# Performance work log

Measured on AMD Instinct MI355X. Metric: run time of the kernel, lower is better.

The kernel has to match this reference:

```python
import jax, jax.numpy as jnp
import numpy as np

WINDOW = (7, 7, 7)
DIM = 192
HEADS = 6
B_ = 256
NW = 32
N = int(np.prod(WINDOW))


def _relative_position_index(window_size):
    coords = np.stack(np.meshgrid(*[np.arange(w) for w in window_size], indexing='ij'))
    cf = coords.reshape(len(window_size), -1)  # (3, N)
    rel = cf[:, :, None] - cf[:, None, :]      # (3, N, N)
    rel = rel.transpose(1, 2, 0).copy()        # (N, N, 3)
    for i, w in enumerate(window_size):
        rel[:, :, i] += w - 1
    rel[:, :, 0] *= (2 * window_size[1] - 1) * (2 * window_size[2] - 1)
    rel[:, :, 1] *= 2 * window_size[2] - 1
    return rel.sum(-1).astype(np.int32)       # (N, N)


def setup_inputs() -> dict:
    key = jax.random.key(0)
    ks = jax.random.split(key, 8)
    table_rows = int(np.prod([2 * w - 1 for w in WINDOW]))  # 2197
    s = 0.02
    return {
        'skip': jax.random.normal(ks[0], (B_, N, DIM), jnp.float32),
        'x_up': jax.random.normal(ks[1], (B_, N, DIM), jnp.float32),
        'mask': jax.random.normal(ks[2], (NW, N, N), jnp.float32),
        'rel_index': jnp.asarray(_relative_position_index(WINDOW)),
        'table': s * jax.random.normal(ks[3], (table_rows, HEADS), jnp.float32),
        'kv_w': jax.random.normal(ks[4], (DIM, 2 * DIM), jnp.float32) / np.sqrt(DIM),
        'kv_b': jnp.zeros((2 * DIM,), jnp.float32),
        'proj_w': jax.random.normal(ks[5], (DIM, DIM), jnp.float32) / np.sqrt(DIM),
        'proj_b': jnp.zeros((DIM,), jnp.float32),
    }


def reference(skip, x_up, mask, rel_index, table, kv_w, kv_b, proj_w, proj_b):
    B, n, C = skip.shape
    H = HEADS
    D = C // H
    scale = D ** -0.5
    # kv projection: (B, N, 2C) -> k, v each (B, H, N, D)
    kv = skip @ kv_w + kv_b
    kv = kv.reshape(B, n, 2, H, D)
    k = kv[:, :, 0].transpose(0, 2, 1, 3)
    v = kv[:, :, 1].transpose(0, 2, 1, 3)
    q = (x_up.reshape(B, n, H, D).transpose(0, 2, 1, 3)) * scale
    attn = jnp.einsum('bhnd,bhmd->bhnm', q, k)  # (B, H, N, N)
    # gathered relative position bias: (N, N, H) -> (H, N, N)
    bias = table[rel_index].transpose(2, 0, 1)
    attn = attn + bias[None]
    nW = mask.shape[0]
    attn = attn.reshape(B // nW, nW, H, n, n) + mask[None, :, None]
    attn = jax.nn.softmax(attn.reshape(B, H, n, n), axis=-1)
    x = jnp.einsum('bhnm,bhmd->bhnd', attn, v)
    x = x.transpose(0, 2, 1, 3).reshape(B, n, C)
    return x @ proj_w + proj_b
```

## Files before the change

kernel.cpp:

```cpp
#include <hip/hip_runtime.h>
#include <hip/hip_bf16.h>

#define B_  256
#define N_  343
#define C_  192
#define H_  6
#define D_  32
#define NW_ 32
#define NN_ (N_*N_)
#define TROWS 2197
#define NP_ 352
#define PLANE (NP_*NP_)

typedef unsigned int  uint32;
typedef unsigned short u16;
typedef __attribute__((ext_vector_type(8))) short bf16x8;
typedef __attribute__((ext_vector_type(4))) float f32x4;

union frag8 { uint4 u4; bf16x8 h8; short s[8]; };

__device__ __forceinline__ float bf2f(u16 u){
  union { uint32 u; float f; } v; v.u = ((uint32)u) << 16; return v.f;
}
__device__ __forceinline__ u16 f2bf(float f){
  union { float f; uint32 u; } v; v.f = f;
  uint32 u = v.u;
  return (u16)((u + 0x7FFFu + ((u >> 16) & 1u)) >> 16);
}

__device__ __forceinline__ bool detect_f32(const uint32* w){
  int c = 0;
  #pragma unroll
  for (int u = 0; u < 32; u++){
    int e = (w[u*37] >> 7) & 0xFF;
    c += (e > 150);
  }
  return c >= 3;
}
__device__ __forceinline__ float ldf(const void* p, size_t i, bool f32){
  return f32 ? ((const float*)p)[i] : bf2f(((const u16*)p)[i]);
}
__device__ __forceinline__ void stf(void* p, size_t i, float v, bool f32){
  if (f32) ((float*)p)[i] = v;
  else     ((u16*)p)[i]   = f2bf(v);
}

__device__ __forceinline__ int klsidx(int j, int d){
  return j*32 + ((((d>>3) ^ ((j>>2)&3)))<<3) + (d&7);
}
__device__ __forceinline__ int vtidx(int d, int j){
  return d*352 + ((((j>>3) ^ ((d>>2)&3)))<<3) + (j&7);
}

__device__ __forceinline__ uint4 ld_row8(const void* __restrict__ src, bool F32,
                                         int b, int grow, int col){
  if (grow >= N_) return make_uint4(0,0,0,0);
  size_t g = ((size_t)b*N_ + grow)*C_ + col;
  if (F32){
    const float* gp = (const float*)src + g;
    float4 f0 = *(const float4*)gp, f1 = *(const float4*)(gp + 4);
    frag8 fv;
    fv.s[0]=(short)f2bf(f0.x); fv.s[1]=(short)f2bf(f0.y);
    fv.s[2]=(short)f2bf(f0.z); fv.s[3]=(short)f2bf(f0.w);
    fv.s[4]=(short)f2bf(f1.x); fv.s[5]=(short)f2bf(f1.y);
    fv.s[6]=(short)f2bf(f1.z); fv.s[7]=(short)f2bf(f1.w);
    return fv.u4;
  }
  return *(const uint4*)((const u16*)src + g);
}


__global__ void prep_bp(const void* __restrict__ skip, const int* __restrict__ rel,
                        const void* __restrict__ table, u16* __restrict__ bp){
  const bool F32 = detect_f32((const uint32*)skip);
  size_t gid = ((size_t)blockIdx.x*256 + threadIdx.x)*8;
  int p   = (int)(gid / PLANE);
  int rem = (int)(gid % PLANE);
  int i = rem / NP_, j0 = rem % NP_;
  frag8 o;
  #pragma unroll
  for (int m = 0; m < 8; m++){
    int j = j0 + m; float v = 0.f;
    if (i < N_ && j < N_){
      int r = rel[i*N_ + j];
      v = ldf(table, (size_t)r*H_ + p, F32);
    }
    o.s[m] = (short)f2bf(v);
  }
  *(uint4*)&bp[gid] = o.u4;
}

__global__ void prep_bm2(const void* __restrict__ skip, const void* __restrict__ mask,
                         const u16* __restrict__ bp, u16* __restrict__ bm){
  const bool F32 = detect_f32((const uint32*)skip);
  const float LOG2E = 1.4426950408889634f;
  size_t gid = ((size_t)blockIdx.x*256 + threadIdx.x)*8;
  int pl  = (int)(gid / PLANE);
  int rem = (int)(gid % PLANE);
  int i = rem / NP_, j0 = rem % NP_;
  int w = pl / H_, h = pl % H_;
  frag8 bg; bg.u4 = *(const uint4*)&bp[(size_t)h*PLANE + rem];
  frag8 o;
  #pragma unroll
  for (int m = 0; m < 8; m++){
    int j = j0 + m;
    float v = bf2f((u16)bg.s[m]);
    if (i < N_ && j < N_) v += ldf(mask, (size_t)w*NN_ + (size_t)i*N_ + j, F32);
    o.s[m] = (short)f2bf(v * LOG2E);
  }
  *(uint4*)&bm[gid] = o.u4;
}

__global__ __launch_bounds__(512, 2) void kv_gemm5(
    const void* __restrict__ skip, const void* __restrict__ kv_w,
    const void* __restrict__ kv_b, u16* __restrict__ kvws){
  __shared__ __align__(16) u16 sk[32*200];
  const bool F32 = detect_f32((const uint32*)skip);
  const int b = blockIdx.x;
  const int t = threadIdx.x, lane = t & 63, wave = t >> 6;
  const int n16 = lane & 15, q = lane >> 4;

  float kvb[3];
  u16*  p3[3];
  int   d3[3], isK[3];
  frag8 bw[3][6];
  #pragma unroll
  for (int c3 = 0; c3 < 3; c3++){
    int col = (wave*3 + c3)*16 + n16;
    kvb[c3] = ldf(kv_b, col, F32);
    #pragma unroll
    for (int ks = 0; ks < 6; ks++)
      #pragma unroll
      for (int j = 0; j < 8; j++)
        bw[c3][ks].s[j] = (short)f2bf(ldf(kv_w, (size_t)(ks*32 + q*8 + j)*384 + col, F32));
    if (col < 192){
      int h = col >> 5; d3[c3] = col & 31; isK[c3] = 1;
      p3[c3] = kvws + (size_t)(b*H_ + h)*22528;
    } else {
      int cv = col - 192; int h = cv >> 5; d3[c3] = cv & 31; isK[c3] = 0;
      p3[c3] = kvws + (size_t)(b*H_ + h)*22528 + 11264;
    }
  }

  const int r0 = t/24,        c0 = (t%24)*8;
  const int r1 = (t+512)/24,  c1 = ((t+512)%24)*8;
  const bool two = (t < 256);
  uint4 pre0 = ld_row8(skip, F32, b, r0, c0);
  uint4 pre1 = two ? ld_row8(skip, F32, b, r1, c1) : make_uint4(0,0,0,0);

  for (int rc = 0; rc < 11; rc++){
    __syncthreads();
    *(uint4*)&sk[r0*200 + c0] = pre0;
    if (two) *(uint4*)&sk[r1*200 + c1] = pre1;
    __syncthreads();
    if (rc < 10){
      int rb = (rc+1)*32;
      pre0 = ld_row8(skip, F32, b, rb + r0, c0);
      if (two) pre1 = ld_row8(skip, F32, b, rb + r1, c1);
    }
    frag8 af[2][6];
    #pragma unroll
    for (int half = 0; half < 2; half++)
      #pragma unroll
      for (int ks = 0; ks < 6; ks++)
        af[half][ks].u4 = *(const uint4*)&sk[(half*16 + n16)*200 + ks*32 + q*8];
    #pragma unroll
    for (int c3 = 0; c3 < 3; c3++){
      #pragma unroll
      for (int half = 0; half < 2; half++){
        f32x4 acc = {0.f,0.f,0.f,0.f};
        #pragma unroll
        for (int ks = 0; ks < 6; ks++)
          acc = __builtin_amdgcn_mfma_f32_16x16x32_bf16(af[half][ks].h8, bw[c3][ks].h8, acc, 0,0,0);
        #pragma unroll
        for (int r = 0; r < 4; r++){
          int grow = rc*32 + half*16 + q*4 + r;
          u16 val = f2bf(acc[r] + kvb[c3]);
          if (isK[c3]) p3[c3][klsidx(grow, d3[c3])] = val;
          else         p3[c3][vtidx(d3[c3], grow)] = val;
        }
      }
    }
  }
}

#define A2_VT  11264
#define A2_TOT 22528

__global__ __launch_bounds__(512, 6) void attn2(
    const void* __restrict__ skip, const void* __restrict__ x_up,
    const u16* __restrict__ bm, const u16* __restrict__ kvws,
    u16* __restrict__ xws, void* __restrict__ out){
  __shared__ __align__(16) u16 sm[A2_TOT];
  const bool F32 = detect_f32((const uint32*)skip);
  const int bid = blockIdx.x;
  const int b = bid / H_, h = bid % H_;
  const int w = b & (NW_-1);
  const int t = threadIdx.x, lane = t & 63, wave = t >> 6;
  const int n16 = lane & 15, q = lane >> 4;

  {
    const uint4* src = (const uint4*)(kvws + (size_t)bid*22528);
    uint4* dst = (uint4*)sm;
    for (int u = t; u < 2816; u += 512) dst[u] = src[u];
  }
  __syncthreads();

  const u16* bmp = bm + (size_t)(w*H_ + h)*PLANE;
  const float SC2 = 0.17677669529663687f * 1.4426950408889634f;
  const int src0 = ((q & 1) << 5) + n16;
  const int src1 = src0 + 16;
  const bool lo = (q < 2);

  for (int it = wave; it < 22; it += 8){
    int i0 = it*16;
    const u16* bmr = bmp + (size_t)(i0 + n16)*NP_;
    frag8 aq;
    {
      int qrow = min(i0 + n16, N_-1);
      size_t base = ((size_t)b*N_ + qrow)*C_ + h*D_ + q*8;
      if (F32){
        const float* xf = (const float*)x_up + base;
        float4 f0 = *(const float4*)xf, f1 = *(const float4*)(xf + 4);
        aq.s[0]=(short)f2bf(f0.x); aq.s[1]=(short)f2bf(f0.y);
        aq.s[2]=(short)f2bf(f0.z); aq.s[3]=(short)f2bf(f0.w);
        aq.s[4]=(short)f2bf(f1.x); aq.s[5]=(short)f2bf(f1.y);
        aq.s[6]=(short)f2bf(f1.z); aq.s[7]=(short)f2bf(f1.w);
      } else {
        aq.u4 = *(const uint4*)((const u16*)x_up + base);
      }
    }
    f32x4 O0 = {0.f,0.f,0.f,0.f}, O1 = {0.f,0.f,0.f,0.f};
    float lp = 0.f;
    for (int jc = 0; jc < 11; jc++){
      int j0 = jc*32;
      uint2 mba = *(const uint2*)&bmr[j0 + q*4];
      uint2 mbb = *(const uint2*)&bmr[j0 + 16 + q*4];
      frag8 bk0, bk1;
      bk0.u4 = *(const uint4*)&sm[klsidx(j0 + n16, q*8)];
      bk1.u4 = *(const uint4*)&sm[klsidx(j0 + 16 + n16, q*8)];
      f32x4 z = {0.f,0.f,0.f,0.f};
      f32x4 s0 = __builtin_amdgcn_mfma_f32_16x16x32_bf16(bk0.h8, aq.h8, z, 0,0,0);
      f32x4 s1 = __builtin_amdgcn_mfma_f32_16x16x32_bf16(bk1.h8, aq.h8, z, 0,0,0);
      union { uint2 v; u16 e[4]; } Ua, Ub;
      Ua.v = mba; Ub.v = mbb;
      float pa[4], pb[4];
      if (jc < 10){
        #pragma unroll
        for (int r = 0; r < 4; r++){
          pa[r] = exp2f(fmaf(s0[r], SC2, bf2f(Ua.e[r])));
          pb[r] = exp2f(fmaf(s1[r], SC2, bf2f(Ub.e[r])));
          lp += pa[r] + pb[r];
        }
      } else {
        #pragma unroll
        for (int r = 0; r < 4; r++){
          pa[r] = exp2f(fmaf(s0[r], SC2, bf2f(Ua.e[r])));
          float eb = exp2f(fmaf(s1[r], SC2, bf2f(Ub.e[r])));
          pb[r] = (336 + q*4 + r < N_) ? eb : 0.f;
          lp += pa[r] + pb[r];
        }
      }
      uint32 A0, A1, B0, B1;
      asm("v_cvt_pk_bf16_f32 %0, %1, %2" : "=v"(A0) : "v"(pa[0]), "v"(pa[1]));
      asm("v_cvt_pk_bf16_f32 %0, %1, %2" : "=v"(A1) : "v"(pa[2]), "v"(pa[3]));
      asm("v_cvt_pk_bf16_f32 %0, %1, %2" : "=v"(B0) : "v"(pb[0]), "v"(pb[1]));
      asm("v_cvt_pk_bf16_f32 %0, %1, %2" : "=v"(B1) : "v"(pb[2]), "v"(pb[3]));
      uint32 a0s = (uint32)__shfl((int)A0, src0), a1s = (uint32)__shfl((int)A1, src0);
      uint32 a2s = (uint32)__shfl((int)A0, src1), a3s = (uint32)__shfl((int)A1, src1);
      uint32 b0s = (uint32)__shfl((int)B0, src0), b1s = (uint32)__shfl((int)B1, src0);
      uint32 b2s = (uint32)__shfl((int)B0, src1), b3s = (uint32)__shfl((int)B1, src1);
      frag8 ap;
      ap.u4.x = lo ? a0s : b0s;
      ap.u4.y = lo ? a1s : b1s;
      ap.u4.z = lo ? a2s : b2s;
      ap.u4.w = lo ? a3s : b3s;
      frag8 bv0, bv1;
      bv0.u4 = *(const uint4*)&sm[A2_VT + vtidx(n16,      j0 + q*8)];
      bv1.u4 = *(const uint4*)&sm[A2_VT + vtidx(16 + n16, j0 + q*8)];
      O0 = __builtin_amdgcn_mfma_f32_16x16x32_bf16(ap.h8, bv0.h8, O0, 0,0,0);
      O1 = __builtin_amdgcn_mfma_f32_16x16x32_bf16(ap.h8, bv1.h8, O1, 0,0,0);
    }
    lp += __shfl_xor(lp, 16);
    lp += __shfl_xor(lp, 32);
    #pragma unroll
    for (int r = 0; r < 4; r++){
      int il = q*4 + r;
      float rl = 1.f / __shfl(lp, (lane & 48) | il);
      int i = i0 + il;
      if (i < N_){
        if (xws){
          u16* xp = xws + ((size_t)(b*H_ + h)*N_ + i)*D_;
          xp[n16]      = f2bf(O0[r]*rl);
          xp[16 + n16] = f2bf(O1[r]*rl);
        } else {
          size_t ob = ((size_t)b*N_ + i)*C_ + h*D_;
          stf(out, ob + n16,      O0[r]*rl, F32);
          stf(out, ob + 16 + n16, O1[r]*rl, F32);
        }
      }
    }
  }
}

__global__ __launch_bounds__(256, 4) void proj4(const u16* __restrict__ xws,
                                                void* __restrict__ outp,
                                                const void* __restrict__ pw,
                                                const void* __restrict__ pb,
                                                const void* __restrict__ skip){
  __shared__ __align__(16) u16 xs[64*200];
  __shared__ __align__(16) float os[16*196];
  const bool F32 = detect_f32((const uint32*)skip);
  const int t = threadIdx.x, lane = t & 63, wave = t >> 6;
  const int n16 = lane & 15, q = lane >> 4;
  const size_t row0 = (size_t)blockIdx.x * 64;

  for (int u = t; u < 1536; u += 256){
    int r = u / 24, c8 = u % 24;
    int g = (int)row0 + r;
    int b = g / N_, i = g - b*N_;
    int h = c8 >> 2, d0 = (c8 & 3)*8;
    uint4 vv = *(const uint4*)&xws[((size_t)(b*H_ + h)*N_ + i)*D_ + d0];
    *(uint4*)&xs[r*200 + h*32 + d0] = vv;
  }
  frag8 bwf[3][6];
  float pbv[3];
  #pragma unroll
  for (int c3 = 0; c3 < 3; c3++){
    int col = (wave*3 + c3)*16 + n16;
    pbv[c3] = ldf(pb, col, F32);
    #pragma unroll
    for (int ks = 0; ks < 6; ks++)
      #pragma unroll
      for (int j = 0; j < 8; j++)
        bwf[c3][ks].s[j] = (short)f2bf(ldf(pw, (size_t)(ks*32 + q*8 + j)*C_ + col, F32));
  }
  __syncthreads();
  for (int rt = 0; rt < 4; rt++){
    frag8 af[6];
    #pragma unroll
    for (int ks = 0; ks < 6; ks++)
      af[ks].u4 = *(const uint4*)&xs[(rt*16 + n16)*200 + ks*32 + q*8];
    #pragma unroll
    for (int c3 = 0; c3 < 3; c3++){
      f32x4 acc = {0.f,0.f,0.f,0.f};
      #pragma unroll
      for (int ks = 0; ks < 6; ks++)
        acc = __builtin_amdgcn_mfma_f32_16x16x32_bf16(af[ks].h8, bwf[c3][ks].h8, acc, 0,0,0);
      int col = (wave*3 + c3)*16 + n16;
      #pragma unroll
      for (int r = 0; r < 4; r++)
        os[(q*4 + r)*196 + col] = acc[r] + pbv[c3];
    }
    __syncthreads();
    size_t rb = row0 + rt*16;
    if (F32){
      for (int u = t; u < 768; u += 256){
        int r = u / 48, c4 = (u % 48)*4;
        *(float4*)((float*)outp + (rb + r)*C_ + c4) = *(const float4*)&os[r*196 + c4];
      }
    } else {
      for (int u = t; u < 384; u += 256){
        int r = u / 24, c8 = (u % 24)*8;
        frag8 o;
        #pragma unroll
        for (int m = 0; m < 8; m++) o.s[m] = (short)f2bf(os[r*196 + c8 + m]);
        *(uint4*)((u16*)outp + (rb + r)*C_ + c8) = o.u4;
      }
    }
    __syncthreads();
  }
}


__global__ void prep_biasg(const void* __restrict__ skip, const int* __restrict__ rel,
                           const void* __restrict__ table, u16* __restrict__ biasg){
  const bool F32 = detect_f32((const uint32*)skip);
  int idx = blockIdx.x*256 + threadIdx.x;
  if (idx >= NN_) return;
  int r = rel[idx];
  #pragma unroll
  for (int h = 0; h < H_; h++)
    biasg[(size_t)h*NN_ + idx] = f2bf(ldf(table, (size_t)r*H_ + h, F32));
}

#define KLS_OFF 6400
#define VT_OFF  (KLS_OFF + 352*40)
#define SMEM_U16 (VT_OFF + 32*360)

__global__ __launch_bounds__(512, 4) void attn_fused(
    const void* __restrict__ skip, const void* __restrict__ x_up,
    const void* __restrict__ mask, const u16* __restrict__ biasg,
    const void* __restrict__ kv_w, const void* __restrict__ kv_b,
    void* __restrict__ out){
  __shared__ __align__(16) u16 sm[SMEM_U16];
  const bool F32 = detect_f32((const uint32*)skip);
  const int bid = blockIdx.x;
  const int b = bid / H_, h = bid % H_;
  const int w = b & (NW_-1);
  const int t = threadIdx.x;
  const int lane = t & 63, wave = t >> 6;
  const int n16 = lane & 15, q = lane >> 4;
  const int colt = wave & 3;
  const int half = wave >> 2;
  const int gcol = (colt < 2) ? (h*D_ + colt*16 + n16)
                              : (C_ + h*D_ + (colt-2)*16 + n16);
  const float kvb = ldf(kv_b, gcol, F32);
  frag8 bw[6];
  #pragma unroll
  for (int ks = 0; ks < 6; ks++)
    #pragma unroll
    for (int j = 0; j < 8; j++)
      bw[ks].s[j] = (short)f2bf(ldf(kv_w, (size_t)(ks*32 + q*8 + j)*384 + gcol, F32));

  for (int rc = 0; rc < 11; rc++){
    __syncthreads();
    for (int u = t; u < 32*C_; u += 512){
      int r = u / C_, c = u % C_;
      int grow = rc*32 + r;
      float v = (grow < N_) ? ldf(skip, ((size_t)b*N_ + grow)*C_ + c, F32) : 0.f;
      sm[r*200 + c] = f2bf(v);
    }
    __syncthreads();
    f32x4 acc = {0.f, 0.f, 0.f, 0.f};
    #pragma unroll
    for (int ks = 0; ks < 6; ks++){
      frag8 a;  a.u4 = *(const uint4*)&sm[(half*16 + n16)*200 + ks*32 + q*8];
      acc = __builtin_amdgcn_mfma_f32_16x16x32_bf16(a.h8, bw[ks].h8, acc, 0, 0, 0);
    }
    #pragma unroll
    for (int r = 0; r < 4; r++){
      int grow = rc*32 + half*16 + q*4 + r;
      u16 val = f2bf(acc[r] + kvb);
      if (colt < 2) sm[KLS_OFF + grow*40 + colt*16 + n16] = val;
      else          sm[VT_OFF + ((colt-2)*16 + n16)*360 + grow] = val;
    }
  }
  __syncthreads();

  const float scale = 0.17677669529663687f;
  const size_t mwb = (size_t)w*NN_;
  const u16* bg = biasg + (size_t)h*NN_;
  u16* pls = &sm[wave*640];
  for (int it = wave; it < 22; it += 8){
    int i0 = it*16;
    {
      int rrow = min(i0 + (lane >> 2), N_-1);
      int col0 = (lane & 3)*8;
      size_t gb = ((size_t)b*N_ + rrow)*C_ + h*D_ + col0;
      u16* dst = &pls[(lane >> 2)*40 + col0];
      #pragma unroll
      for (int m = 0; m < 8; m++) dst[m] = f2bf(ldf(x_up, gb + m, F32) * scale);
    }
    frag8 aq; aq.u4 = *(const uint4*)&pls[n16*40 + q*8];
    f32x4 O0 = {0.f,0.f,0.f,0.f}, O1 = {0.f,0.f,0.f,0.f};
    float lp[4] = {0.f, 0.f, 0.f, 0.f};
    int ic[4];
    #pragma unroll
    for (int r = 0; r < 4; r++) ic[r] = min(i0 + q*4 + r, N_-1);
    for (int jc = 0; jc < 11; jc++){
      int j0 = jc*32;
      int ja = j0 + n16, jb = j0 + 16 + n16;
      int jac = min(ja, N_-1), jbc = min(jb, N_-1);
      float bma[4], bmb[4];
      #pragma unroll
      for (int r = 0; r < 4; r++){
        size_t rb = (size_t)ic[r]*N_;
        bma[r] = bf2f(bg[rb + jac]) + ldf(mask, mwb + rb + jac, F32);
        bmb[r] = bf2f(bg[rb + jbc]) + ldf(mask, mwb + rb + jbc, F32);
      }
      frag8 bk0, bk1;
      bk0.u4 = *(const uint4*)&sm[KLS_OFF + (j0 + n16)*40 + q*8];
      bk1.u4 = *(const uint4*)&sm[KLS_OFF + (j0 + 16 + n16)*40 + q*8];
      f32x4 z = {0.f,0.f,0.f,0.f};
      f32x4 s0 = __builtin_amdgcn_mfma_f32_16x16x32_bf16(aq.h8, bk0.h8, z, 0,0,0);
      f32x4 s1 = __builtin_amdgcn_mfma_f32_16x16x32_bf16(aq.h8, bk1.h8, z, 0,0,0);
      #pragma unroll
      for (int r = 0; r < 4; r++){
        float pa = (ja < N_) ? __expf(s0[r] + bma[r] - 12.f) : 0.f;
        float pb = (jb < N_) ? __expf(s1[r] + bmb[r] - 12.f) : 0.f;
        lp[r] += pa + pb;
        pls[(q*4 + r)*40 + n16]      = f2bf(pa);
        pls[(q*4 + r)*40 + 16 + n16] = f2bf(pb);
      }
      frag8 ap; ap.u4 = *(const uint4*)&pls[n16*40 + q*8];
      frag8 bv0, bv1;
      bv0.u4 = *(const uint4*)&sm[VT_OFF + n16*360 + j0 + q*8];
      bv1.u4 = *(const uint4*)&sm[VT_OFF + (16 + n16)*360 + j0 + q*8];
      O0 = __builtin_amdgcn_mfma_f32_16x16x32_bf16(ap.h8, bv0.h8, O0, 0,0,0);
      O1 = __builtin_amdgcn_mfma_f32_16x16x32_bf16(ap.h8, bv1.h8, O1, 0,0,0);
    }
    #pragma unroll
    for (int msk = 1; msk < 16; msk <<= 1){
      #pragma unroll
      for (int r = 0; r < 4; r++) lp[r] += __shfl_xor(lp[r], msk, 64);
    }
    #pragma unroll
    for (int r = 0; r < 4; r++){
      int i = i0 + q*4 + r;
      if (i < N_){
        float rl = 1.f / lp[r];
        size_t ob = ((size_t)b*N_ + i)*C_ + h*D_;
        stf(out, ob + n16,      O0[r]*rl, F32);
        stf(out, ob + 16 + n16, O1[r]*rl, F32);
      }
    }
  }
}

__global__ __launch_bounds__(256, 6) void proj2(void* __restrict__ io,
                                                const void* __restrict__ pw,
                                                const void* __restrict__ pb,
                                                const void* __restrict__ skip){
  __shared__ __align__(16) u16 xs[64*200];
  const bool F32 = detect_f32((const uint32*)skip);
  const int t = threadIdx.x;
  const int lane = t & 63, wave = t >> 6;
  const int n16 = lane & 15, q = lane >> 4;
  const size_t row0 = (size_t)blockIdx.x * 64;

  for (int u = t; u < 64*C_/8; u += 256){
    int r = u / 24, c = (u % 24)*8;
    size_t g = (row0 + r)*C_ + c;
    uint4 vv;
    if (F32){
      const float* gp = (const float*)io + g;
      float4 f0 = *(const float4*)gp, f1 = *(const float4*)(gp + 4);
      frag8 fv;
      fv.s[0]=(short)f2bf(f0.x); fv.s[1]=(short)f2bf(f0.y);
      fv.s[2]=(short)f2bf(f0.z); fv.s[3]=(short)f2bf(f0.w);
      fv.s[4]=(short)f2bf(f1.x); fv.s[5]=(short)f2bf(f1.y);
      fv.s[6]=(short)f2bf(f1.z); fv.s[7]=(short)f2bf(f1.w);
      vv = fv.u4;
    } else {
      vv = *(const uint4*)((const u16*)io + g);
    }
    *(uint4*)&xs[r*200 + c] = vv;
  }
  __syncthreads();
  for (int c3 = 0; c3 < 3; c3++){
    int col = (wave*3 + c3)*16 + n16;
    float pbv = ldf(pb, col, F32);
    frag8 bwf[6];
    #pragma unroll
    for (int ks = 0; ks < 6; ks++)
      #pragma unroll
      for (int j = 0; j < 8; j++)
        bwf[ks].s[j] = (short)f2bf(ldf(pw, (size_t)(ks*32 + q*8 + j)*C_ + col, F32));
    for (int rt = 0; rt < 4; rt++){
      frag8 af[6];
      #pragma unroll
      for (int ks = 0; ks < 6; ks++)
        af[ks].u4 = *(const uint4*)&xs[(rt*16 + n16)*200 + ks*32 + q*8];
      f32x4 acc = {0.f,0.f,0.f,0.f};
      #pragma unroll
      for (int ks = 0; ks < 6; ks++)
        acc = __builtin_amdgcn_mfma_f32_16x16x32_bf16(af[ks].h8, bwf[ks].h8, acc, 0,0,0);
      #pragma unroll
      for (int r = 0; r < 4; r++)
        stf(io, (row0 + rt*16 + q*4 + r)*C_ + col, acc[r] + pbv, F32);
    }
  }
}

extern "C" void kernel_launch(void* const* d_in, const int* in_sizes, int n_in,
                              void* d_out, int out_size, void* d_ws, size_t ws_size,
                              hipStream_t stream){
  (void)in_sizes; (void)n_in; (void)out_size;
  const void* skip  = d_in[0];
  const void* x_up  = d_in[1];
  const void* mask  = d_in[2];
  const int*  rel   = (const int*)d_in[3];
  const void* table = d_in[4];
  const void* kv_w  = d_in[5];
  const void* kv_b  = d_in[6];
  const void* pw    = d_in[7];
  const void* pb    = d_in[8];

  const size_t BM_BYTES = (size_t)192*PLANE*2;
  const size_t KV_BYTES = (size_t)B_*H_*45056;
  const size_t BP_BYTES = (size_t)H_*PLANE*2;
  const size_t XW_BYTES = (size_t)B_*H_*N_*D_*2;

  if (ws_size >= BM_BYTES + KV_BYTES + XW_BYTES){
    u16* bm   = (u16*)d_ws;
    u16* kvws = (u16*)((char*)d_ws + BM_BYTES);
    u16* xws  = (u16*)((char*)d_ws + BM_BYTES + KV_BYTES);
    u16* bp   = xws;
    prep_bp <<<(H_*PLANE/8)/256, 256, 0, stream>>>(skip, rel, table, bp);
    prep_bm2<<<(192*PLANE/8)/256, 256, 0, stream>>>(skip, mask, bp, bm);
    kv_gemm5<<<B_, 512, 0, stream>>>(skip, kv_w, kv_b, kvws);
    attn2   <<<B_*H_, 512, 0, stream>>>(skip, x_up, bm, kvws, xws, d_out);
    proj4   <<<87808/64, 256, 0, stream>>>(xws, d_out, pw, pb, skip);
  } else if (ws_size >= BM_BYTES + KV_BYTES + BP_BYTES){
    u16* bm   = (u16*)d_ws;
    u16* kvws = (u16*)((char*)d_ws + BM_BYTES);
    u16* bp   = (u16*)((char*)d_ws + BM_BYTES + KV_BYTES);
    prep_bp <<<(H_*PLANE/8)/256, 256, 0, stream>>>(skip, rel, table, bp);
    prep_bm2<<<(192*PLANE/8)/256, 256, 0, stream>>>(skip, mask, bp, bm);
    kv_gemm5<<<B_, 512, 0, stream>>>(skip, kv_w, kv_b, kvws);
    attn2   <<<B_*H_, 512, 0, stream>>>(skip, x_up, bm, kvws, nullptr, d_out);
    proj2   <<<87808/64, 256, 0, stream>>>(d_out, pw, pb, skip);
  } else {
    u16* biasg = (u16*)d_ws;
    prep_biasg<<<(NN_+255)/256, 256, 0, stream>>>(skip, rel, table, biasg);
    attn_fused<<<B_*H_, 512, 0, stream>>>(skip, x_up, mask, biasg, kv_w, kv_b, d_out);
    proj2     <<<87808/64, 256, 0, stream>>>(d_out, pw, pb, skip);
  }
}
```

Before: 422.0 us.

## Store bias and mask planes separately instead of precombined per head-window

Drops the 192-plane precombined bias+mask buffer and writes 6 bias planes plus 32 mask planes in a single prep kernel. The attention kernel loads both and adds them before the exp. This removes one prep launch and cuts the write and read volume of the combined buffer, and the smaller footprint is more likely to stay in cache. The cost is a second global load stream and one extra add per score in the attention inner loop, plus a small rounding difference from summing two bf16 values instead of rounding once.

```diff
diff --git a/kernel.cpp b/kernel.cpp
--- a/kernel.cpp
+++ b/kernel.cpp
@@ -70,45 +70,38 @@
 }
 
 
-__global__ void prep_bp(const void* __restrict__ skip, const int* __restrict__ rel,
-                        const void* __restrict__ table, u16* __restrict__ bp){
+#define PM_PLANES (H_ + NW_)
+__global__ void prep_pm(const void* __restrict__ skip, const int* __restrict__ rel,
+                        const void* __restrict__ table, const void* __restrict__ mask,
+                        u16* __restrict__ pm){
   const bool F32 = detect_f32((const uint32*)skip);
+  const float LOG2E = 1.4426950408889634f;
   size_t gid = ((size_t)blockIdx.x*256 + threadIdx.x)*8;
   int p   = (int)(gid / PLANE);
   int rem = (int)(gid % PLANE);
   int i = rem / NP_, j0 = rem % NP_;
   frag8 o;
-  #pragma unroll
-  for (int m = 0; m < 8; m++){
-    int j = j0 + m; float v = 0.f;
-    if (i < N_ && j < N_){
-      int r = rel[i*N_ + j];
-      v = ldf(table, (size_t)r*H_ + p, F32);
-    }
-    o.s[m] = (short)f2bf(v);
-  }
-  *(uint4*)&bp[gid] = o.u4;
-}
-
-__global__ void prep_bm2(const void* __restrict__ skip, const void* __restrict__ mask,
-                         const u16* __restrict__ bp, u16* __restrict__ bm){
-  const bool F32 = detect_f32((const uint32*)skip);
-  const float LOG2E = 1.4426950408889634f;
-  size_t gid = ((size_t)blockIdx.x*256 + threadIdx.x)*8;
-  int pl  = (int)(gid / PLANE);
-  int rem = (int)(gid % PLANE);
-  int i = rem / NP_, j0 = rem % NP_;
-  int w = pl / H_, h = pl % H_;
-  frag8 bg; bg.u4 = *(const uint4*)&bp[(size_t)h*PLANE + rem];
-  frag8 o;
-  #pragma unroll
-  for (int m = 0; m < 8; m++){
-    int j = j0 + m;
-    float v = bf2f((u16)bg.s[m]);
-    if (i < N_ && j < N_) v += ldf(mask, (size_t)w*NN_ + (size_t)i*N_ + j, F32);
-    o.s[m] = (short)f2bf(v * LOG2E);
-  }
-  *(uint4*)&bm[gid] = o.u4;
+  if (p < H_){
+    #pragma unroll
+    for (int m = 0; m < 8; m++){
+      int j = j0 + m; float v = 0.f;
+      if (i < N_ && j < N_){
+        int r = rel[i*N_ + j];
+        v = ldf(table, (size_t)r*H_ + p, F32) * LOG2E;
+      }
+      o.s[m] = (short)f2bf(v);
+    }
+  } else {
+    int w = p - H_;
+    #pragma unroll
+    for (int m = 0; m < 8; m++){
+      int j = j0 + m; float v = 0.f;
+      if (i < N_ && j < N_)
+        v = ldf(mask, (size_t)w*NN_ + (size_t)i*N_ + j, F32) * LOG2E;
+      o.s[m] = (short)f2bf(v);
+    }
+  }
+  *(uint4*)&pm[gid] = o.u4;
 }
 
 __global__ __launch_bounds__(512, 2) void kv_gemm5(
@@ -189,7 +182,8 @@
 
 __global__ __launch_bounds__(512, 6) void attn2(
     const void* __restrict__ skip, const void* __restrict__ x_up,
-    const u16* __restrict__ bm, const u16* __restrict__ kvws,
+    const u16* __restrict__ bp, const u16* __restrict__ msp,
+    const u16* __restrict__ kvws,
     u16* __restrict__ xws, void* __restrict__ out){
   __shared__ __align__(16) u16 sm[A2_TOT];
   const bool F32 = detect_f32((const uint32*)skip);
@@ -206,7 +200,8 @@
   }
   __syncthreads();
 
-  const u16* bmp = bm + (size_t)(w*H_ + h)*PLANE;
+  const u16* bpl = bp  + (size_t)h*PLANE;
+  const u16* mpl = msp + (size_t)w*PLANE;
   const float SC2 = 0.17677669529663687f * 1.4426950408889634f;
   const int src0 = ((q & 1) << 5) + n16;
   const int src1 = src0 + 16;
@@ -214,7 +209,8 @@
 
   for (int it = wave; it < 22; it += 8){
     int i0 = it*16;
-    const u16* bmr = bmp + (size_t)(i0 + n16)*NP_;
+    const u16* br = bpl + (size_t)(i0 + n16)*NP_;
+    const u16* mr = mpl + (size_t)(i0 + n16)*NP_;
     frag8 aq;
     {
       int qrow = min(i0 + n16, N_-1);
@@ -234,29 +230,30 @@
     float lp = 0.f;
     for (int jc = 0; jc < 11; jc++){
       int j0 = jc*32;
-      uint2 mba = *(const uint2*)&bmr[j0 + q*4];
-      uint2 mbb = *(const uint2*)&bmr[j0 + 16 + q*4];
+      union U4 { uint2 v; u16 e[4]; } Ba, Bb, Ma, Mb;
+      Ba.v = *(const uint2*)&br[j0 + q*4];
+      Bb.v = *(const uint2*)&br[j0 + 16 + q*4];
+      Ma.v = *(const uint2*)&mr[j0 + q*4];
+      Mb.v = *(const uint2*)&mr[j0 + 16 + q*4];
       frag8 bk0, bk1;
       bk0.u4 = *(const uint4*)&sm[klsidx(j0 + n16, q*8)];
       bk1.u4 = *(const uint4*)&sm[klsidx(j0 + 16 + n16, q*8)];
       f32x4 z = {0.f,0.f,0.f,0.f};
       f32x4 s0 = __builtin_amdgcn_mfma_f32_16x16x32_bf16(bk0.h8, aq.h8, z, 0,0,0);
       f32x4 s1 = __builtin_amdgcn_mfma_f32_16x16x32_bf16(bk1.h8, aq.h8, z, 0,0,0);
-      union { uint2 v; u16 e[4]; } Ua, Ub;
-      Ua.v = mba; Ub.v = mbb;
       float pa[4], pb[4];
       if (jc < 10){
         #pragma unroll
         for (int r = 0; r < 4; r++){
-          pa[r] = exp2f(fmaf(s0[r], SC2, bf2f(Ua.e[r])));
-          pb[r] = exp2f(fmaf(s1[r], SC2, bf2f(Ub.e[r])));
+          pa[r] = exp2f(fmaf(s0[r], SC2, bf2f(Ba.e[r]) + bf2f(Ma.e[r])));
+          pb[r] = exp2f(fmaf(s1[r], SC2, bf2f(Bb.e[r]) + bf2f(Mb.e[r])));
           lp += pa[r] + pb[r];
         }
       } else {
         #pragma unroll
         for (int r = 0; r < 4; r++){
-          pa[r] = exp2f(fmaf(s0[r], SC2, bf2f(Ua.e[r])));
-          float eb = exp2f(fmaf(s1[r], SC2, bf2f(Ub.e[r])));
+          pa[r] = exp2f(fmaf(s0[r], SC2, bf2f(Ba.e[r]) + bf2f(Ma.e[r])));
+          float eb = exp2f(fmaf(s1[r], SC2, bf2f(Bb.e[r]) + bf2f(Mb.e[r])));
           pb[r] = (336 + q*4 + r < N_) ? eb : 0.f;
           lp += pa[r] + pb[r];
         }
@@ -577,29 +574,28 @@
   const void* pw    = d_in[7];
   const void* pb    = d_in[8];
 
-  const size_t BM_BYTES = (size_t)192*PLANE*2;
+  const size_t PM_BYTES = (size_t)PM_PLANES*PLANE*2;
   const size_t KV_BYTES = (size_t)B_*H_*45056;
-  const size_t BP_BYTES = (size_t)H_*PLANE*2;
   const size_t XW_BYTES = (size_t)B_*H_*N_*D_*2;
 
-  if (ws_size >= BM_BYTES + KV_BYTES + XW_BYTES){
-    u16* bm   = (u16*)d_ws;
-    u16* kvws = (u16*)((char*)d_ws + BM_BYTES);
-    u16* xws  = (u16*)((char*)d_ws + BM_BYTES + KV_BYTES);
-    u16* bp   = xws;
-    prep_bp <<<(H_*PLANE/8)/256, 256, 0, stream>>>(skip, rel, table, bp);
-    prep_bm2<<<(192*PLANE/8)/256, 256, 0, stream>>>(skip, mask, bp, bm);
+  if (ws_size >= PM_BYTES + KV_BYTES + XW_BYTES){
+    u16* pm   = (u16*)d_ws;
+    u16* bpp  = pm;
+    u16* msp  = pm + (size_t)H_*PLANE;
+    u16* kvws = (u16*)((char*)d_ws + PM_BYTES);
+    u16* xws  = (u16*)((char*)d_ws + PM_BYTES + KV_BYTES);
+    prep_pm <<<(PM_PLANES*PLANE/8)/256, 256, 0, stream>>>(skip, rel, table, mask, pm);
     kv_gemm5<<<B_, 512, 0, stream>>>(skip, kv_w, kv_b, kvws);
-    attn2   <<<B_*H_, 512, 0, stream>>>(skip, x_up, bm, kvws, xws, d_out);
+    attn2   <<<B_*H_, 512, 0, stream>>>(skip, x_up, bpp, msp, kvws, xws, d_out);
     proj4   <<<87808/64, 256, 0, stream>>>(xws, d_out, pw, pb, skip);
-  } else if (ws_size >= BM_BYTES + KV_BYTES + BP_BYTES){
-    u16* bm   = (u16*)d_ws;
-    u16* kvws = (u16*)((char*)d_ws + BM_BYTES);
-    u16* bp   = (u16*)((char*)d_ws + BM_BYTES + KV_BYTES);
-    prep_bp <<<(H_*PLANE/8)/256, 256, 0, stream>>>(skip, rel, table, bp);
-    prep_bm2<<<(192*PLANE/8)/256, 256, 0, stream>>>(skip, mask, bp, bm);
+  } else if (ws_size >= PM_BYTES + KV_BYTES){
+    u16* pm   = (u16*)d_ws;
+    u16* bpp  = pm;
+    u16* msp  = pm + (size_t)H_*PLANE;
+    u16* kvws = (u16*)((char*)d_ws + PM_BYTES);
+    prep_pm <<<(PM_PLANES*PLANE/8)/256, 256, 0, stream>>>(skip, rel, table, mask, pm);
     kv_gemm5<<<B_, 512, 0, stream>>>(skip, kv_w, kv_b, kvws);
-    attn2   <<<B_*H_, 512, 0, stream>>>(skip, x_up, bm, kvws, nullptr, d_out);
+    attn2   <<<B_*H_, 512, 0, stream>>>(skip, x_up, bpp, msp, kvws, nullptr, d_out);
     proj2   <<<87808/64, 256, 0, stream>>>(d_out, pw, pb, skip);
   } else {
     u16* biasg = (u16*)d_ws;
```

Result: faster. 412.3 us (-2.3%).
